# Kernel tuning notes

Hardware: AMD Instinct MI355X
Metric: run time of the kernel (lower is better)

The kernel has to match this reference:

```python
import jax, jax.numpy as jnp
import numpy as np

N = 1024
D = 128            # hidden_dim
TEMPERATURE = 1.0
SPARSE_K = 32


def setup_inputs() -> dict:
    key = jax.random.key(0)
    ks = jax.random.split(key, 10)
    s = 1.0 / np.sqrt(D)
    s2 = 1.0 / np.sqrt(2 * D)
    z = jax.random.normal(ks[0], (N, D), dtype=jnp.float32)
    spatial_dist = jax.random.uniform(ks[1], (N, N), dtype=jnp.float32)
    # Linear weights stored as [in, out] (transposed vs torch) so y = x @ W + b
    Wq = jax.random.normal(ks[2], (D, D), dtype=jnp.float32) * s
    bq = jnp.zeros((D,), dtype=jnp.float32)
    Wk = jax.random.normal(ks[3], (D, D), dtype=jnp.float32) * s
    bk = jnp.zeros((D,), dtype=jnp.float32)
    W1 = jax.random.normal(ks[4], (2 * D, D), dtype=jnp.float32) * s2
    b1 = jnp.zeros((D,), dtype=jnp.float32)
    W2 = jax.random.normal(ks[5], (D, 3), dtype=jnp.float32) * s
    b2 = jnp.zeros((3,), dtype=jnp.float32)
    return {"z": z, "spatial_dist": spatial_dist, "Wq": Wq, "bq": bq,
            "Wk": Wk, "bk": bk, "W1": W1, "b1": b1, "W2": W2, "b2": b2}


def reference(z, spatial_dist, Wq, bq, Wk, bk, W1, b1, W2, b2):
    n = z.shape[0]
    # ---- attention adjacency ----
    Q = z @ Wq + bq                                   # [N, D]
    K = z @ Wk + bk                                   # [N, D]
    attn = (Q @ K.T) * (1.0 / (D ** 0.5)) / TEMPERATURE   # [N, N]
    attn = attn * jnp.exp(-spatial_dist)              # spatial weighting
    adjacency = jax.nn.softmax(attn, axis=-1)
    # top-k sparsification (scatter top-k values into zeros)
    topk_vals, topk_idx = jax.lax.top_k(adjacency, SPARSE_K)   # [N, k]
    rows = jnp.arange(n)[:, None]
    adjacency = jnp.zeros_like(adjacency).at[rows, topk_idx].set(topk_vals)
    # ---- pairwise signaling-type classifier ----
    a = z @ W1[:D]                                    # [N, D]
    b = z @ W1[D:]                                    # [N, D]
    h = jax.nn.gelu(a[:, None, :] + b[None, :, :] + b1, approximate=False)  # [N, N, D]
    logits = jnp.einsum('ijd,dc->ijc', h, W2) + b2    # [N, N, 3]
    signaling_type = jax.nn.softmax(logits, axis=-1)
    return adjacency, signaling_type
```

## Files before the change

### kernel.cpp

```cpp
#include <hip/hip_runtime.h>
#include <hip/hip_fp16.h>

#define N 1024
#define D 128

__global__ __launch_bounds__(256) void proj_kernel(
    const float* __restrict__ z,
    const float* __restrict__ Wq, const float* __restrict__ bq,
    const float* __restrict__ Wk, const float* __restrict__ bk,
    const float* __restrict__ W1, const float* __restrict__ b1,
    float* __restrict__ Q, float* __restrict__ Kx,
    __half* __restrict__ Ah, __half* __restrict__ Bh)
{
    const int d  = threadIdx.x & (D - 1);
    const int h  = threadIdx.x >> 7;
    const int r0 = blockIdx.x * 8;
    const float* __restrict__ Wa = h ? W1           : Wq;
    const float* __restrict__ Wb = h ? (W1 + D * D) : Wk;

    float acc0[8] = {0,0,0,0,0,0,0,0};
    float acc1[8] = {0,0,0,0,0,0,0,0};

    for (int c = 0; c < D / 4; ++c) {
        float4 zr[8];
#pragma unroll
        for (int r = 0; r < 8; ++r)
            zr[r] = *(const float4*)&z[(r0 + r) * D + c * 4];
#pragma unroll
        for (int q = 0; q < 4; ++q) {
            const int k = c * 4 + q;
            const float wa = Wa[k * D + d];
            const float wb = Wb[k * D + d];
#pragma unroll
            for (int r = 0; r < 8; ++r) {
                const float zv = (q == 0) ? zr[r].x : (q == 1) ? zr[r].y : (q == 2) ? zr[r].z : zr[r].w;
                acc0[r] = fmaf(zv, wa, acc0[r]);
                acc1[r] = fmaf(zv, wb, acc1[r]);
            }
        }
    }
    if (h == 0) {
        const float c0 = bq[d], c1 = bk[d];
        const float scale = 0.08838834764831845f;
#pragma unroll
        for (int r = 0; r < 8; ++r) {
            Q [(r0 + r) * D + d] = (acc0[r] + c0) * scale;
            Kx[(r0 + r) * D + d] = acc1[r] + c1;
        }
    } else {
        const float c0 = b1[d];
#pragma unroll
        for (int r = 0; r < 8; ++r) {
            Ah[(r0 + r) * D + d] = __float2half(acc0[r] + c0);
            Bh[(r0 + r) * D + d] = __float2half(acc1[r]);
        }
    }
}

__global__ __launch_bounds__(256) void score_kernel(
    const float* __restrict__ Q, const float* __restrict__ Kx,
    const float* __restrict__ dist, float* __restrict__ S)
{
    __shared__ float Qs[32 * 33 * 4];
    __shared__ float Ks[32 * 33 * 4];
    const int tid = threadIdx.x;
    const int bi = blockIdx.y * 32, bj = blockIdx.x * 32;
    const int tx = tid & 15, ty = tid >> 4;

#pragma unroll
    for (int t = 0; t < 4; ++t) {
        const int e = t * 256 + tid;
        const int row = e >> 5, c = e & 31;
        *(float4*)&Qs[(row * 33 + c) * 4] = *(const float4*)&Q [(size_t)(bi + row) * D + c * 4];
        *(float4*)&Ks[(row * 33 + c) * 4] = *(const float4*)&Kx[(size_t)(bj + row) * D + c * 4];
    }
    __syncthreads();

    const float4* Qs4 = (const float4*)Qs;
    const float4* Ks4 = (const float4*)Ks;
    float a00 = 0.f, a01 = 0.f, a10 = 0.f, a11 = 0.f;

#pragma unroll 4
    for (int c = 0; c < 32; ++c) {
        const float4 q0 = Qs4[ty * 33 + c];
        const float4 q1 = Qs4[(ty + 16) * 33 + c];
        const float4 k0 = Ks4[tx * 33 + c];
        const float4 k1 = Ks4[(tx + 16) * 33 + c];
        a00 = fmaf(q0.x, k0.x, a00); a00 = fmaf(q0.y, k0.y, a00); a00 = fmaf(q0.z, k0.z, a00); a00 = fmaf(q0.w, k0.w, a00);
        a01 = fmaf(q0.x, k1.x, a01); a01 = fmaf(q0.y, k1.y, a01); a01 = fmaf(q0.z, k1.z, a01); a01 = fmaf(q0.w, k1.w, a01);
        a10 = fmaf(q1.x, k0.x, a10); a10 = fmaf(q1.y, k0.y, a10); a10 = fmaf(q1.z, k0.z, a10); a10 = fmaf(q1.w, k0.w, a10);
        a11 = fmaf(q1.x, k1.x, a11); a11 = fmaf(q1.y, k1.y, a11); a11 = fmaf(q1.z, k1.z, a11); a11 = fmaf(q1.w, k1.w, a11);
    }

    const int i0 = bi + ty, i1 = bi + ty + 16;
    const int j0 = bj + tx, j1 = bj + tx + 16;
    S[(size_t)i0 * N + j0] = a00 * __expf(-dist[(size_t)i0 * N + j0]);
    S[(size_t)i0 * N + j1] = a01 * __expf(-dist[(size_t)i0 * N + j1]);
    S[(size_t)i1 * N + j0] = a10 * __expf(-dist[(size_t)i1 * N + j0]);
    S[(size_t)i1 * N + j1] = a11 * __expf(-dist[(size_t)i1 * N + j1]);
}

__global__ __launch_bounds__(256) void topk_kernel(float* buf)
{
    const int lane = threadIdx.x & 63;
    const int row  = blockIdx.x * 4 + (threadIdx.x >> 6);
    float* sr = buf + (size_t)row * N;

    float v[16];
#pragma unroll
    for (int c = 0; c < 4; ++c) {
        const float4 f = *(const float4*)&sr[(c * 64 + lane) * 4];
        v[c * 4 + 0] = f.x; v[c * 4 + 1] = f.y; v[c * 4 + 2] = f.z; v[c * 4 + 3] = f.w;
    }
    float m = v[0];
#pragma unroll
    for (int e = 1; e < 16; ++e) m = fmaxf(m, v[e]);
#pragma unroll
    for (int off = 1; off < 64; off <<= 1) m = fmaxf(m, __shfl_xor(m, off));
    float sum = 0.f;
#pragma unroll
    for (int e = 0; e < 16; ++e) sum += __expf(v[e] - m);
#pragma unroll
    for (int off = 1; off < 64; off <<= 1) sum += __shfl_xor(sum, off);
    const float inv = 1.0f / sum;

    unsigned long long key[16];
#pragma unroll
    for (int e = 0; e < 16; ++e) {
        const int j = (((e >> 2) * 64 + lane) * 4) + (e & 3);
        unsigned u = __float_as_uint(v[e]);
        u = (u & 0x80000000u) ? ~u : (u | 0x80000000u);
        key[e] = ((unsigned long long)u << 32) | (unsigned)(N - 1 - j);
    }
    unsigned flags = 0;
    for (int it = 0; it < 32; ++it) {
        unsigned long long best = key[0];
#pragma unroll
        for (int e = 1; e < 16; ++e) best = (key[e] > best) ? key[e] : best;
#pragma unroll
        for (int off = 1; off < 64; off <<= 1) {
            const unsigned long long o = __shfl_xor(best, off);
            if (o > best) best = o;
        }
#pragma unroll
        for (int e = 0; e < 16; ++e)
            if (key[e] == best) { flags |= 1u << e; key[e] = 0ull; }
    }
#pragma unroll
    for (int c = 0; c < 4; ++c) {
        float4 o;
        o.x = (flags & (1u << (c * 4 + 0))) ? __expf(v[c * 4 + 0] - m) * inv : 0.f;
        o.y = (flags & (1u << (c * 4 + 1))) ? __expf(v[c * 4 + 1] - m) * inv : 0.f;
        o.z = (flags & (1u << (c * 4 + 2))) ? __expf(v[c * 4 + 2] - m) * inv : 0.f;
        o.w = (flags & (1u << (c * 4 + 3))) ? __expf(v[c * 4 + 3] - m) * inv : 0.f;
        *(float4*)&sr[(c * 64 + lane) * 4] = o;
    }
}

union H2x4 { uint4 u; __half2 h[4]; };

__device__ __forceinline__ float fdot2_acc(__half2 a, __half2 b, float c) {
#if __has_builtin(__builtin_amdgcn_fdot2)
    typedef _Float16 v2h __attribute__((ext_vector_type(2)));
    union { __half2 h; v2h v; } ua, ub;
    ua.h = a; ub.h = b;
    return __builtin_amdgcn_fdot2(ua.v, ub.v, c, false);
#else
    return fmaf(__low2float(a), __low2float(b),
           fmaf(__high2float(a), __high2float(b), c));
#endif
}

#define HP 136

__global__ __launch_bounds__(256) void pair_kernel(
    const __half* __restrict__ Ah, const __half* __restrict__ Bh,
    const float* __restrict__ W2, const float* __restrict__ b2,
    float* __restrict__ out)
{
    __shared__ __align__(16) __half AsH[32 * HP];
    __shared__ __align__(16) __half BsH[32 * HP];
    __shared__ __align__(16) __half2 Wh[3][68];
    const int tid = threadIdx.x;
    const int bi = blockIdx.y * 32, bj = blockIdx.x * 32;
    const int tx = tid & 15, ty = tid >> 4;

#pragma unroll
    for (int t = 0; t < 2; ++t) {
        const int e = t * 256 + tid;
        const int row = e >> 4, c = e & 15;
        *(uint4*)&AsH[row * HP + c * 8] = *(const uint4*)&Ah[(size_t)(bi + row) * D + c * 8];
        *(uint4*)&BsH[row * HP + c * 8] = *(const uint4*)&Bh[(size_t)(bj + row) * D + c * 8];
    }
    if (tid < 192) {
        const int cls = tid >> 6, dp = tid & 63;
        Wh[cls][dp] = __floats2half2_rn(W2[6 * dp + cls], W2[6 * dp + 3 + cls]);
    }
    const float bb0 = b2[0], bb1 = b2[1], bb2 = b2[2];
    __syncthreads();

    float acc[4][3];
#pragma unroll
    for (int p = 0; p < 4; ++p) { acc[p][0] = bb0; acc[p][1] = bb1; acc[p][2] = bb2; }

    const __half2 C3  = __float2half2_rn(-0.1029434f);
    const __half2 C1  = __float2half2_rn(-2.3022082f);
    const __half2 ONE = __float2half2_rn(1.0f);

#pragma unroll 4
    for (int c = 0; c < 16; ++c) {
        H2x4 a0, a1, b0, b1, w0, w1, w2;
        a0.u = *(const uint4*)&AsH[ty * HP + c * 8];
        a1.u = *(const uint4*)&AsH[(ty + 16) * HP + c * 8];
        b0.u = *(const uint4*)&BsH[tx * HP + c * 8];
        b1.u = *(const uint4*)&BsH[(tx + 16) * HP + c * 8];
        w0.u = *(const uint4*)&Wh[0][c * 4];
        w1.u = *(const uint4*)&Wh[1][c * 4];
        w2.u = *(const uint4*)&Wh[2][c * 4];
#pragma unroll
        for (int dp = 0; dp < 4; ++dp) {
            const __half2 aa[2] = { a0.h[dp], a1.h[dp] };
            const __half2 bb[2] = { b0.h[dp], b1.h[dp] };
            const __half2 wc0 = w0.h[dp], wc1 = w1.h[dp], wc2 = w2.h[dp];
#pragma unroll
            for (int ii = 0; ii < 2; ++ii)
#pragma unroll
                for (int jj = 0; jj < 2; ++jj) {
                    const __half2 x = __hadd2(aa[ii], bb[jj]);
                    const __half2 u = __hmul2(x, x);
                    const __half2 p = __hfma2(C3, u, C1);
                    const __half2 t = __hmul2(x, p);
                    const __half2 e = h2exp2(t);
                    const __half2 dn = __hadd2(e, ONE);
                    const __half2 r = h2rcp(dn);
                    const __half2 g = __hmul2(x, r);
                    float* l = acc[ii * 2 + jj];
                    l[0] = fdot2_acc(g, wc0, l[0]);
                    l[1] = fdot2_acc(g, wc1, l[1]);
                    l[2] = fdot2_acc(g, wc2, l[2]);
                }
        }
    }

#pragma unroll
    for (int ii = 0; ii < 2; ++ii)
#pragma unroll
        for (int jj = 0; jj < 2; ++jj) {
            const int i = bi + ty + 16 * ii;
            const int j = bj + tx + 16 * jj;
            const float* l = acc[ii * 2 + jj];
            const float mm = fmaxf(l[0], fmaxf(l[1], l[2]));
            const float e0 = __expf(l[0] - mm), e1 = __expf(l[1] - mm), e2 = __expf(l[2] - mm);
            const float inv2 = 1.0f / (e0 + e1 + e2);
            float* o = out + ((size_t)i * N + j) * 3;
            o[0] = e0 * inv2; o[1] = e1 * inv2; o[2] = e2 * inv2;
        }
}

extern "C" void kernel_launch(void* const* d_in, const int* in_sizes, int n_in,
                              void* d_out, int out_size, void* d_ws, size_t ws_size,
                              hipStream_t stream)
{
    const float* z    = (const float*)d_in[0];
    const float* dist = (const float*)d_in[1];
    const float* Wq   = (const float*)d_in[2];
    const float* bq   = (const float*)d_in[3];
    const float* Wk   = (const float*)d_in[4];
    const float* bk   = (const float*)d_in[5];
    const float* W1   = (const float*)d_in[6];
    const float* b1   = (const float*)d_in[7];
    const float* W2   = (const float*)d_in[8];
    const float* b2   = (const float*)d_in[9];

    float* out = (float*)d_out;
    float* ws  = (float*)d_ws;
    float*  Q  = ws;
    float*  K  = ws + (size_t)N * D;
    __half* Ah = (__half*)(ws + 2 * (size_t)N * D);
    __half* Bh = Ah + (size_t)N * D;

    proj_kernel<<<N / 8, 256, 0, stream>>>(z, Wq, bq, Wk, bk, W1, b1, Q, K, Ah, Bh);
    score_kernel<<<dim3(N / 32, N / 32), 256, 0, stream>>>(Q, K, dist, out);
    topk_kernel<<<N / 4, 256, 0, stream>>>(out);
    pair_kernel<<<dim3(N / 32, N / 32), 256, 0, stream>>>(Ah, Bh, W2, b2, out + (size_t)N * N);
}
```

Before: 160.5 us.

## Use fp16 Q/K with fdot2, 32-bit topk keys, and drop one logit class

Q and K are stored as fp16 and the score dot products use packed fdot2, halving shared memory and load traffic. The top-k selection packs a truncated 22-bit value and the index into 32-bit keys, replacing 64-bit compares and shuffles. The pair classifier subtracts the third class's weights so only two dot products per element are needed, with the third logit fixed at zero. The projection kernel uses fewer rows per block for more parallelism. Risks: fp16 score precision and truncated keys may change top-k selection on near-ties.

Measured after the change: 142.9 us. 1.12x faster.

```diff
diff --git a/kernel.cpp b/kernel.cpp
--- a/kernel.cpp
+++ b/kernel.cpp
@@ -9,22 +9,22 @@
     const float* __restrict__ Wq, const float* __restrict__ bq,
     const float* __restrict__ Wk, const float* __restrict__ bk,
     const float* __restrict__ W1, const float* __restrict__ b1,
-    float* __restrict__ Q, float* __restrict__ Kx,
+    __half* __restrict__ Qh, __half* __restrict__ Kh,
     __half* __restrict__ Ah, __half* __restrict__ Bh)
 {
     const int d  = threadIdx.x & (D - 1);
     const int h  = threadIdx.x >> 7;
-    const int r0 = blockIdx.x * 8;
+    const int r0 = blockIdx.x * 4;
     const float* __restrict__ Wa = h ? W1           : Wq;
     const float* __restrict__ Wb = h ? (W1 + D * D) : Wk;
 
-    float acc0[8] = {0,0,0,0,0,0,0,0};
-    float acc1[8] = {0,0,0,0,0,0,0,0};
+    float acc0[4] = {0,0,0,0};
+    float acc1[4] = {0,0,0,0};
 
     for (int c = 0; c < D / 4; ++c) {
-        float4 zr[8];
-#pragma unroll
-        for (int r = 0; r < 8; ++r)
+        float4 zr[4];
+#pragma unroll
+        for (int r = 0; r < 4; ++r)
             zr[r] = *(const float4*)&z[(r0 + r) * D + c * 4];
 #pragma unroll
         for (int q = 0; q < 4; ++q) {
@@ -32,7 +32,7 @@
             const float wa = Wa[k * D + d];
             const float wb = Wb[k * D + d];
 #pragma unroll
-            for (int r = 0; r < 8; ++r) {
+            for (int r = 0; r < 4; ++r) {
                 const float zv = (q == 0) ? zr[r].x : (q == 1) ? zr[r].y : (q == 2) ? zr[r].z : zr[r].w;
                 acc0[r] = fmaf(zv, wa, acc0[r]);
                 acc1[r] = fmaf(zv, wb, acc1[r]);
@@ -43,117 +43,17 @@
         const float c0 = bq[d], c1 = bk[d];
         const float scale = 0.08838834764831845f;
 #pragma unroll
-        for (int r = 0; r < 8; ++r) {
-            Q [(r0 + r) * D + d] = (acc0[r] + c0) * scale;
-            Kx[(r0 + r) * D + d] = acc1[r] + c1;
+        for (int r = 0; r < 4; ++r) {
+            Qh[(r0 + r) * D + d] = __float2half((acc0[r] + c0) * scale);
+            Kh[(r0 + r) * D + d] = __float2half(acc1[r] + c1);
         }
     } else {
         const float c0 = b1[d];
 #pragma unroll
-        for (int r = 0; r < 8; ++r) {
+        for (int r = 0; r < 4; ++r) {
             Ah[(r0 + r) * D + d] = __float2half(acc0[r] + c0);
             Bh[(r0 + r) * D + d] = __float2half(acc1[r]);
         }
-    }
-}
-
-__global__ __launch_bounds__(256) void score_kernel(
-    const float* __restrict__ Q, const float* __restrict__ Kx,
-    const float* __restrict__ dist, float* __restrict__ S)
-{
-    __shared__ float Qs[32 * 33 * 4];
-    __shared__ float Ks[32 * 33 * 4];
-    const int tid = threadIdx.x;
-    const int bi = blockIdx.y * 32, bj = blockIdx.x * 32;
-    const int tx = tid & 15, ty = tid >> 4;
-
-#pragma unroll
-    for (int t = 0; t < 4; ++t) {
-        const int e = t * 256 + tid;
-        const int row = e >> 5, c = e & 31;
-        *(float4*)&Qs[(row * 33 + c) * 4] = *(const float4*)&Q [(size_t)(bi + row) * D + c * 4];
-        *(float4*)&Ks[(row * 33 + c) * 4] = *(const float4*)&Kx[(size_t)(bj + row) * D + c * 4];
-    }
-    __syncthreads();
-
-    const float4* Qs4 = (const float4*)Qs;
-    const float4* Ks4 = (const float4*)Ks;
-    float a00 = 0.f, a01 = 0.f, a10 = 0.f, a11 = 0.f;
-
-#pragma unroll 4
-    for (int c = 0; c < 32; ++c) {
-        const float4 q0 = Qs4[ty * 33 + c];
-        const float4 q1 = Qs4[(ty + 16) * 33 + c];
-        const float4 k0 = Ks4[tx * 33 + c];
-        const float4 k1 = Ks4[(tx + 16) * 33 + c];
-        a00 = fmaf(q0.x, k0.x, a00); a00 = fmaf(q0.y, k0.y, a00); a00 = fmaf(q0.z, k0.z, a00); a00 = fmaf(q0.w, k0.w, a00);
-        a01 = fmaf(q0.x, k1.x, a01); a01 = fmaf(q0.y, k1.y, a01); a01 = fmaf(q0.z, k1.z, a01); a01 = fmaf(q0.w, k1.w, a01);
-        a10 = fmaf(q1.x, k0.x, a10); a10 = fmaf(q1.y, k0.y, a10); a10 = fmaf(q1.z, k0.z, a10); a10 = fmaf(q1.w, k0.w, a10);
-        a11 = fmaf(q1.x, k1.x, a11); a11 = fmaf(q1.y, k1.y, a11); a11 = fmaf(q1.z, k1.z, a11); a11 = fmaf(q1.w, k1.w, a11);
-    }
-
-    const int i0 = bi + ty, i1 = bi + ty + 16;
-    const int j0 = bj + tx, j1 = bj + tx + 16;
-    S[(size_t)i0 * N + j0] = a00 * __expf(-dist[(size_t)i0 * N + j0]);
-    S[(size_t)i0 * N + j1] = a01 * __expf(-dist[(size_t)i0 * N + j1]);
-    S[(size_t)i1 * N + j0] = a10 * __expf(-dist[(size_t)i1 * N + j0]);
-    S[(size_t)i1 * N + j1] = a11 * __expf(-dist[(size_t)i1 * N + j1]);
-}
-
-__global__ __launch_bounds__(256) void topk_kernel(float* buf)
-{
-    const int lane = threadIdx.x & 63;
-    const int row  = blockIdx.x * 4 + (threadIdx.x >> 6);
-    float* sr = buf + (size_t)row * N;
-
-    float v[16];
-#pragma unroll
-    for (int c = 0; c < 4; ++c) {
-        const float4 f = *(const float4*)&sr[(c * 64 + lane) * 4];
-        v[c * 4 + 0] = f.x; v[c * 4 + 1] = f.y; v[c * 4 + 2] = f.z; v[c * 4 + 3] = f.w;
-    }
-    float m = v[0];
-#pragma unroll
-    for (int e = 1; e < 16; ++e) m = fmaxf(m, v[e]);
-#pragma unroll
-    for (int off = 1; off < 64; off <<= 1) m = fmaxf(m, __shfl_xor(m, off));
-    float sum = 0.f;
-#pragma unroll
-    for (int e = 0; e < 16; ++e) sum += __expf(v[e] - m);
-#pragma unroll
-    for (int off = 1; off < 64; off <<= 1) sum += __shfl_xor(sum, off);
-    const float inv = 1.0f / sum;
-
-    unsigned long long key[16];
-#pragma unroll
-    for (int e = 0; e < 16; ++e) {
-        const int j = (((e >> 2) * 64 + lane) * 4) + (e & 3);
-        unsigned u = __float_as_uint(v[e]);
-        u = (u & 0x80000000u) ? ~u : (u | 0x80000000u);
-        key[e] = ((unsigned long long)u << 32) | (unsigned)(N - 1 - j);
-    }
-    unsigned flags = 0;
-    for (int it = 0; it < 32; ++it) {
-        unsigned long long best = key[0];
-#pragma unroll
-        for (int e = 1; e < 16; ++e) best = (key[e] > best) ? key[e] : best;
-#pragma unroll
-        for (int off = 1; off < 64; off <<= 1) {
-            const unsigned long long o = __shfl_xor(best, off);
-            if (o > best) best = o;
-        }
-#pragma unroll
-        for (int e = 0; e < 16; ++e)
-            if (key[e] == best) { flags |= 1u << e; key[e] = 0ull; }
-    }
-#pragma unroll
-    for (int c = 0; c < 4; ++c) {
-        float4 o;
-        o.x = (flags & (1u << (c * 4 + 0))) ? __expf(v[c * 4 + 0] - m) * inv : 0.f;
-        o.y = (flags & (1u << (c * 4 + 1))) ? __expf(v[c * 4 + 1] - m) * inv : 0.f;
-        o.z = (flags & (1u << (c * 4 + 2))) ? __expf(v[c * 4 + 2] - m) * inv : 0.f;
-        o.w = (flags & (1u << (c * 4 + 3))) ? __expf(v[c * 4 + 3] - m) * inv : 0.f;
-        *(float4*)&sr[(c * 64 + lane) * 4] = o;
     }
 }
 
@@ -173,6 +73,108 @@
 
 #define HP 136
 
+__global__ __launch_bounds__(256) void score_kernel(
+    const __half* __restrict__ Qh, const __half* __restrict__ Kh,
+    const float* __restrict__ dist, float* __restrict__ S)
+{
+    __shared__ __align__(16) __half Qs[32 * HP];
+    __shared__ __align__(16) __half Ks[32 * HP];
+    const int tid = threadIdx.x;
+    const int bi = blockIdx.y * 32, bj = blockIdx.x * 32;
+    const int tx = tid & 15, ty = tid >> 4;
+
+#pragma unroll
+    for (int t = 0; t < 2; ++t) {
+        const int e = t * 256 + tid;
+        const int row = e >> 4, c = e & 15;
+        *(uint4*)&Qs[row * HP + c * 8] = *(const uint4*)&Qh[(size_t)(bi + row) * D + c * 8];
+        *(uint4*)&Ks[row * HP + c * 8] = *(const uint4*)&Kh[(size_t)(bj + row) * D + c * 8];
+    }
+    __syncthreads();
+
+    float a00 = 0.f, a01 = 0.f, a10 = 0.f, a11 = 0.f;
+
+#pragma unroll 4
+    for (int c = 0; c < 16; ++c) {
+        H2x4 q0, q1, k0, k1;
+        q0.u = *(const uint4*)&Qs[ty * HP + c * 8];
+        q1.u = *(const uint4*)&Qs[(ty + 16) * HP + c * 8];
+        k0.u = *(const uint4*)&Ks[tx * HP + c * 8];
+        k1.u = *(const uint4*)&Ks[(tx + 16) * HP + c * 8];
+#pragma unroll
+        for (int dp = 0; dp < 4; ++dp) {
+            a00 = fdot2_acc(q0.h[dp], k0.h[dp], a00);
+            a01 = fdot2_acc(q0.h[dp], k1.h[dp], a01);
+            a10 = fdot2_acc(q1.h[dp], k0.h[dp], a10);
+            a11 = fdot2_acc(q1.h[dp], k1.h[dp], a11);
+        }
+    }
+
+    const int i0 = bi + ty, i1 = bi + ty + 16;
+    const int j0 = bj + tx, j1 = bj + tx + 16;
+    S[(size_t)i0 * N + j0] = a00 * __expf(-dist[(size_t)i0 * N + j0]);
+    S[(size_t)i0 * N + j1] = a01 * __expf(-dist[(size_t)i0 * N + j1]);
+    S[(size_t)i1 * N + j0] = a10 * __expf(-dist[(size_t)i1 * N + j0]);
+    S[(size_t)i1 * N + j1] = a11 * __expf(-dist[(size_t)i1 * N + j1]);
+}
+
+__global__ __launch_bounds__(256) void topk_kernel(float* buf)
+{
+    const int lane = threadIdx.x & 63;
+    const int row  = blockIdx.x * 4 + (threadIdx.x >> 6);
+    float* sr = buf + (size_t)row * N;
+
+    float v[16];
+#pragma unroll
+    for (int c = 0; c < 4; ++c) {
+        const float4 f = *(const float4*)&sr[(c * 64 + lane) * 4];
+        v[c * 4 + 0] = f.x; v[c * 4 + 1] = f.y; v[c * 4 + 2] = f.z; v[c * 4 + 3] = f.w;
+    }
+    float m = v[0];
+#pragma unroll
+    for (int e = 1; e < 16; ++e) m = fmaxf(m, v[e]);
+#pragma unroll
+    for (int off = 1; off < 64; off <<= 1) m = fmaxf(m, __shfl_xor(m, off));
+    float sum = 0.f;
+#pragma unroll
+    for (int e = 0; e < 16; ++e) sum += __expf(v[e] - m);
+#pragma unroll
+    for (int off = 1; off < 64; off <<= 1) sum += __shfl_xor(sum, off);
+    const float inv = 1.0f / sum;
+
+    unsigned key[16];
+#pragma unroll
+    for (int e = 0; e < 16; ++e) {
+        const int j = (((e >> 2) * 64 + lane) * 4) + (e & 3);
+        unsigned u = __float_as_uint(v[e]);
+        u = (u & 0x80000000u) ? ~u : (u | 0x80000000u);
+        key[e] = (u & 0xFFFFFC00u) | (unsigned)(N - 1 - j);
+    }
+    unsigned flags = 0;
+    for (int it = 0; it < 32; ++it) {
+        unsigned best = key[0];
+#pragma unroll
+        for (int e = 1; e < 16; ++e) best = (key[e] > best) ? key[e] : best;
+#pragma unroll
+        for (int off = 1; off < 64; off <<= 1) {
+            const unsigned o = __shfl_xor(best, off);
+            if (o > best) best = o;
+        }
+#pragma unroll
+        for (int e = 0; e < 16; ++e)
+            if (key[e] == best) { flags |= 1u << e; key[e] = 0u; }
+    }
+#pragma unroll
+    for (int c = 0; c < 4; ++c) {
+        float4 o;
+        o.x = (flags & (1u << (c * 4 + 0))) ? __expf(v[c * 4 + 0] - m) * inv : 0.f;
+        o.y = (flags & (1u << (c * 4 + 1))) ? __expf(v[c * 4 + 1] - m) * inv : 0.f;
+        o.z = (flags & (1u << (c * 4 + 2))) ? __expf(v[c * 4 + 2] - m) * inv : 0.f;
+        o.w = (flags & (1u << (c * 4 + 3))) ? __expf(v[c * 4 + 3] - m) * inv : 0.f;
+        *(float4*)&sr[(c * 64 + lane) * 4] = o;
+    }
+}
+
 __global__ __launch_bounds__(256) void pair_kernel(
     const __half* __restrict__ Ah, const __half* __restrict__ Bh,
     const float* __restrict__ W2, const float* __restrict__ b2,
@@ -180,7 +182,7 @@
 {
     __shared__ __align__(16) __half AsH[32 * HP];
     __shared__ __align__(16) __half BsH[32 * HP];
-    __shared__ __align__(16) __half2 Wh[3][68];
+    __shared__ __align__(16) __half2 Wh[2][68];
     const int tid = threadIdx.x;
     const int bi = blockIdx.y * 32, bj = blockIdx.x * 32;
     const int tx = tid & 15, ty = tid >> 4;
@@ -192,16 +194,17 @@
         *(uint4*)&AsH[row * HP + c * 8] = *(const uint4*)&Ah[(size_t)(bi + row) * D + c * 8];
         *(uint4*)&BsH[row * HP + c * 8] = *(const uint4*)&Bh[(size_t)(bj + row) * D + c * 8];
     }
-    if (tid < 192) {
+    if (tid < 128) {
         const int cls = tid >> 6, dp = tid & 63;
-        Wh[cls][dp] = __floats2half2_rn(W2[6 * dp + cls], W2[6 * dp + 3 + cls]);
-    }
-    const float bb0 = b2[0], bb1 = b2[1], bb2 = b2[2];
+        Wh[cls][dp] = __floats2half2_rn(W2[6 * dp + cls]     - W2[6 * dp + 2],
+                                        W2[6 * dp + 3 + cls] - W2[6 * dp + 5]);
+    }
+    const float bb0 = b2[0] - b2[2], bb1 = b2[1] - b2[2];
     __syncthreads();
 
-    float acc[4][3];
-#pragma unroll
-    for (int p = 0; p < 4; ++p) { acc[p][0] = bb0; acc[p][1] = bb1; acc[p][2] = bb2; }
+    float acc[4][2];
+#pragma unroll
+    for (int p = 0; p < 4; ++p) { acc[p][0] = bb0; acc[p][1] = bb1; }
 
     const __half2 C3  = __float2half2_rn(-0.1029434f);
     const __half2 C1  = __float2half2_rn(-2.3022082f);
@@ -209,19 +212,18 @@
 
 #pragma unroll 4
     for (int c = 0; c < 16; ++c) {
-        H2x4 a0, a1, b0, b1, w0, w1, w2;
+        H2x4 a0, a1, b0, b1, w0, w1;
         a0.u = *(const uint4*)&AsH[ty * HP + c * 8];
         a1.u = *(const uint4*)&AsH[(ty + 16) * HP + c * 8];
         b0.u = *(const uint4*)&BsH[tx * HP + c * 8];
         b1.u = *(const uint4*)&BsH[(tx + 16) * HP + c * 8];
         w0.u = *(const uint4*)&Wh[0][c * 4];
         w1.u = *(const uint4*)&Wh[1][c * 4];
-        w2.u = *(const uint4*)&Wh[2][c * 4];
 #pragma unroll
         for (int dp = 0; dp < 4; ++dp) {
             const __half2 aa[2] = { a0.h[dp], a1.h[dp] };
             const __half2 bb[2] = { b0.h[dp], b1.h[dp] };
-            const __half2 wc0 = w0.h[dp], wc1 = w1.h[dp], wc2 = w2.h[dp];
+            const __half2 wc0 = w0.h[dp], wc1 = w1.h[dp];
 #pragma unroll
             for (int ii = 0; ii < 2; ++ii)
 #pragma unroll
@@ -237,7 +239,6 @@
                     float* l = acc[ii * 2 + jj];
                     l[0] = fdot2_acc(g, wc0, l[0]);
                     l[1] = fdot2_acc(g, wc1, l[1]);
-                    l[2] = fdot2_acc(g, wc2, l[2]);
                 }
         }
     }
@@ -249,8 +250,9 @@
             const int i = bi + ty + 16 * ii;
             const int j = bj + tx + 16 * jj;
             const float* l = acc[ii * 2 + jj];
-            const float mm = fmaxf(l[0], fmaxf(l[1], l[2]));
-            const float e0 = __expf(l[0] - mm), e1 = __expf(l[1] - mm), e2 = __expf(l[2] - mm);
+            const float l0 = l[0], l1 = l[1];
+            const float mm = fmaxf(fmaxf(l0, l1), 0.f);
+            const float e0 = __expf(l0 - mm), e1 = __expf(l1 - mm), e2 = __expf(-mm);
             const float inv2 = 1.0f / (e0 + e1 + e2);
             float* o = out + ((size_t)i * N + j) * 3;
             o[0] = e0 * inv2; o[1] = e1 * inv2; o[2] = e2 * inv2;
@@ -273,14 +275,13 @@
     const float* b2   = (const float*)d_in[9];
 
     float* out = (float*)d_out;
-    float* ws  = (float*)d_ws;
-    float*  Q  = ws;
-    float*  K  = ws + (size_t)N * D;
-    __half* Ah = (__half*)(ws + 2 * (size_t)N * D);
+    __half* Qh = (__half*)d_ws;
+    __half* Kh = Qh + (size_t)N * D;
+    __half* Ah = Kh + (size_t)N * D;
     __half* Bh = Ah + (size_t)N * D;
 
-    proj_kernel<<<N / 8, 256, 0, stream>>>(z, Wq, bq, Wk, bk, W1, b1, Q, K, Ah, Bh);
-    score_kernel<<<dim3(N / 32, N / 32), 256, 0, stream>>>(Q, K, dist, out);
+    proj_kernel<<<N / 4, 256, 0, stream>>>(z, Wq, bq, Wk, bk, W1, b1, Qh, Kh, Ah, Bh);
+    score_kernel<<<dim3(N / 32, N / 32), 256, 0, stream>>>(Qh, Kh, dist, out);
     topk_kernel<<<N / 4, 256, 0, stream>>>(out);
     pair_kernel<<<dim3(N / 32, N / 32), 256, 0, stream>>>(Ah, Bh, W2, b2, out + (size_t)N * N);
 }
```
